# Optimization experiments

Hardware: AMD Instinct MI355X
Metric: run time of the kernel (lower is better)

The kernel has to match this reference:

```python
import jax, jax.numpy as jnp
import numpy as np

NUM_HEADS = 12
HEAD_DIM = 128
HIDDEN = 1536
SCALE = HEAD_DIM ** -0.5


def apply_rope(x, rope):
    # x: [B,H,S,D], rope: [S,1,D] -> freqs [S,D]
    freqs = rope[:, 0, :]
    cos = jnp.repeat(freqs[:, 0::2], 2, axis=-1)[None, None]  # [1,1,S,D]
    sin = jnp.repeat(freqs[:, 1::2], 2, axis=-1)[None, None]
    xr = x.reshape(*x.shape[:-1], -1, 2)
    x_real, x_imag = xr[..., 0], xr[..., 1]
    x_rot = jnp.stack([-x_imag, x_real], axis=-1).reshape(x.shape)
    return x * cos + x_rot * sin


def qkv_split(x, W):
    # x: [B,S,hidden], W: [3*H*D, hidden] (torch Linear layout)
    B, S, _ = x.shape
    y = (x @ W.T).reshape(B, S, 3, NUM_HEADS, HEAD_DIM).transpose(2, 0, 3, 1, 4)
    return y[0], y[1], y[2]  # each [B,H,S,D]


def sdpa(q, k, v):
    s = jnp.einsum('bhqd,bhkd->bhqk', q, k) * SCALE
    p = jax.nn.softmax(s, axis=-1)
    return jnp.einsum('bhqk,bhkd->bhqd', p, v)


def setup_inputs() -> dict:
    key = jax.random.key(0)
    ks = jax.random.split(key, 7)
    B, L, N = 1, 512, 4096
    txt = jax.random.normal(ks[0], (B, L, HIDDEN), dtype=jnp.float32)
    img = jax.random.normal(ks[1], (B, N, HIDDEN), dtype=jnp.float32)
    rope = jax.random.uniform(ks[2], (N, 1, HEAD_DIM), dtype=jnp.float32)
    s = 0.02
    W_txt_qkv = jax.random.normal(ks[3], (3 * NUM_HEADS * HEAD_DIM, HIDDEN), dtype=jnp.float32) * s
    W_img_qkv = jax.random.normal(ks[4], (3 * NUM_HEADS * HEAD_DIM, HIDDEN), dtype=jnp.float32) * s
    W_txt_out = jax.random.normal(ks[5], (HIDDEN, NUM_HEADS * HEAD_DIM), dtype=jnp.float32) * s
    W_img_out = jax.random.normal(ks[6], (HIDDEN, NUM_HEADS * HEAD_DIM), dtype=jnp.float32) * s
    return {'txt': txt, 'img': img, 'rope': rope, 'W_txt_qkv': W_txt_qkv,
            'W_img_qkv': W_img_qkv, 'W_txt_out': W_txt_out, 'W_img_out': W_img_out}


def reference(txt, img, rope, W_txt_qkv, W_img_qkv, W_txt_out, W_img_out):
    B, L, _ = txt.shape
    _, N, _ = img.shape
    txt_q, txt_k, txt_v = qkv_split(txt, W_txt_qkv)
    img_q, img_k, img_v = qkv_split(img, W_img_qkv)
    img_q = apply_rope(img_q, rope)
    img_k = apply_rope(img_k, rope)
    k = jnp.concatenate([txt_k, img_k], axis=2)  # [B,H,L+N,D]
    v = jnp.concatenate([txt_v, img_v], axis=2)
    txt_o = sdpa(txt_q, k, v).transpose(0, 2, 1, 3).reshape(B, L, -1)
    img_o = sdpa(img_q, k, v).transpose(0, 2, 1, 3).reshape(B, N, -1)
    return txt_o @ W_txt_out.T, img_o @ W_img_out.T
```

## Files before the change

### kernel.cpp

```cpp
#include <hip/hip_runtime.h>
#include <hip/hip_bf16.h>
#include <stdint.h>


typedef __attribute__((ext_vector_type(8)))  short bf16x8;
typedef __attribute__((ext_vector_type(4)))  float f32x4;
typedef __attribute__((ext_vector_type(16))) float f32x16;
typedef __attribute__((ext_vector_type(4)))  short s16x4;

#define NUM_HEADS 12
#define HEAD_DIM  128
#define HIDDEN    1536
#define LTXT      512
#define NIMG      4096
#define STOT      4608
#define QKV3      4608
#define SCALE_Q2  (0.08838834764831845f * 1.44269504088896340f)
#define DEFER_THR 12.0f

__device__ __forceinline__ float b2f(short s) {
    union { uint32_t u; float f; } c; c.u = ((uint32_t)(uint16_t)s) << 16; return c.f;
}
__device__ __forceinline__ short f2b(float f) {
    union { float f; uint32_t u; } c; c.f = f;
    uint32_t u = c.u + 0x7FFFu + ((c.u >> 16) & 1u);
    return (short)(u >> 16);
}
__device__ __forceinline__ float fexp2(float x) {
#if __has_builtin(__builtin_amdgcn_exp2f)
    return __builtin_amdgcn_exp2f(x);
#else
    return exp2f(x);
#endif
}
__device__ __forceinline__ uint32_t cvt_pk_bf16(float lo, float hi) {
    uint32_t r;
    asm("v_cvt_pk_bf16_f32 %0, %1, %2" : "=v"(r) : "v"(lo), "v"(hi));
    return r;
}
__device__ __forceinline__ void permlane32_swap(uint32_t& a, uint32_t& b) {
    asm("v_permlane32_swap_b32 %0, %1" : "+v"(a), "+v"(b));
}

typedef const void __attribute__((address_space(1)))* gas_p;
typedef void __attribute__((address_space(3)))* las_p;
__device__ __forceinline__ void gload_lds16(const void* g, void* l) {
    __builtin_amdgcn_global_load_lds((gas_p)g, (las_p)l, 16, 0, 0);
}

__global__ __launch_bounds__(256) void cast6(
    const float* __restrict__ s0, const float* __restrict__ s1,
    const float* __restrict__ s2, const float* __restrict__ s3,
    const float* __restrict__ s4, const float* __restrict__ s5,
    short* __restrict__ dst)
{
    size_t i = (size_t)blockIdx.x * 256 + threadIdx.x;
    const size_t e0 = 98304, e1 = 884736, e2 = 1769472,
                 e3 = 2654208, e4 = 2949120;
    const float* src; size_t base;
    if (i < e2) {
        if (i < e0)      { src = s0; base = 0;  }
        else if (i < e1) { src = s1; base = e0; }
        else             { src = s2; base = e1; }
    } else {
        if (i < e3)      { src = s3; base = e2; }
        else if (i < e4) { src = s4; base = e3; }
        else             { src = s5; base = e4; }
    }
    const float4* p = (const float4*)src + (i - base) * 2;
    float4 a = p[0], b = p[1];
    bf16x8 o;
    o[0] = f2b(a.x); o[1] = f2b(a.y); o[2] = f2b(a.z); o[3] = f2b(a.w);
    o[4] = f2b(b.x); o[5] = f2b(b.y); o[6] = f2b(b.z); o[7] = f2b(b.w);
    *((bf16x8*)dst + i) = o;
}

template <typename OT>
__global__ __launch_bounds__(256) void gemm_bt2(
    const short* __restrict__ A, const short* __restrict__ B0,
    const short* __restrict__ B1, OT* __restrict__ C,
    int M, int N, int K, int rowsplit)
{
    __shared__ __align__(16) short As[2][128 * 32];
    __shared__ __align__(16) short Bs[2][128 * 32];
    const int t    = threadIdx.x;
    const int lane = t & 63, wid = t >> 6;
    const int wr = wid >> 1, wc = wid & 1;
    const int l15 = lane & 15, lk = lane >> 4;
    const int bm = blockIdx.y, bn = blockIdx.x;

    const short* B = (bm * 128 < rowsplit) ? B0 : B1;
    const int srow = t >> 2, skg = t & 3;
    const short* Ag = A + (size_t)(bm * 128 + srow) * K + skg * 8;
    const short* Bg = B + (size_t)(bn * 128 + srow) * K + skg * 8;
    const size_t rowblk = (size_t)64 * K;

    f32x4 acc[4][4];
    const f32x4 z = {0.f, 0.f, 0.f, 0.f};
#pragma unroll
    for (int i = 0; i < 4; ++i)
#pragma unroll
        for (int j = 0; j < 4; ++j) acc[i][j] = z;

    auto STAGE = [&](int b, int kt) {
        const int k0 = kt * 32;
        gload_lds16(Ag + k0,          &As[b][wid * 512]);
        gload_lds16(Ag + rowblk + k0, &As[b][2048 + wid * 512]);
        gload_lds16(Bg + k0,          &Bs[b][wid * 512]);
        gload_lds16(Bg + rowblk + k0, &Bs[b][2048 + wid * 512]);
    };

    const int NT = K / 32;
    STAGE(0, 0);
    for (int kt = 0; kt < NT; ++kt) {
        const int cur = kt & 1;
        if (kt + 1 < NT) {
            STAGE(cur ^ 1, kt + 1);
            asm volatile("s_waitcnt vmcnt(4)" ::: "memory");
        } else {
            asm volatile("s_waitcnt vmcnt(0)" ::: "memory");
        }
        __builtin_amdgcn_s_barrier();

        bf16x8 af[4], bfr[4];
#pragma unroll
        for (int i = 0; i < 4; ++i)
            af[i] = *(const bf16x8*)&As[cur][(wr * 64 + i * 16 + l15) * 32 + lk * 8];
#pragma unroll
        for (int j = 0; j < 4; ++j)
            bfr[j] = *(const bf16x8*)&Bs[cur][(wc * 64 + j * 16 + l15) * 32 + lk * 8];
        __builtin_amdgcn_s_setprio(1);
#pragma unroll
        for (int i = 0; i < 4; ++i)
#pragma unroll
            for (int j = 0; j < 4; ++j)
                acc[i][j] = __builtin_amdgcn_mfma_f32_16x16x32_bf16(
                    af[i], bfr[j], acc[i][j], 0, 0, 0);
        __builtin_amdgcn_s_setprio(0);

        asm volatile("s_waitcnt lgkmcnt(0)" ::: "memory");
        __builtin_amdgcn_sched_barrier(0);
        __builtin_amdgcn_s_barrier();
    }

#pragma unroll
    for (int i = 0; i < 4; ++i) {
#pragma unroll
        for (int j = 0; j < 4; ++j) {
            const int row0 = bm * 128 + wr * 64 + i * 16 + lk * 4;
            const int col  = bn * 128 + wc * 64 + j * 16 + l15;
#pragma unroll
            for (int r = 0; r < 4; ++r) {
                float v = acc[i][j][r];
                if constexpr (sizeof(OT) == 2)
                    C[(size_t)(row0 + r) * N + col] = (OT)f2b(v);
                else
                    C[(size_t)(row0 + r) * N + col] = v;
            }
        }
    }
}

__global__ __launch_bounds__(256) void pack_qkv(
    const short* __restrict__ Y, const float* __restrict__ rope,
    short* __restrict__ Qb, short* __restrict__ Kb, short* __restrict__ VTb)
{
    const int st = blockIdx.x, h = blockIdx.y, t = threadIdx.x;
    const int s0 = st * 64;
    __shared__ __align__(16) short Vt[128][72];

#pragma unroll
    for (int i = 0; i < 4; ++i) {
        int e  = t + i * 256;
        int sl = e >> 4, dg = e & 15;
        int s  = s0 + sl;
        const short* src = Y + (size_t)s * QKV3;
        bf16x8 q8 = *(const bf16x8*)(src + h * 128 + dg * 8);
        bf16x8 k8 = *(const bf16x8*)(src + (12 + h) * 128 + dg * 8);
        bf16x8 v8 = *(const bf16x8*)(src + (24 + h) * 128 + dg * 8);
        float qf[8], kf[8];
#pragma unroll
        for (int j = 0; j < 8; ++j) { qf[j] = b2f(q8[j]); kf[j] = b2f(k8[j]); }
        if (s >= LTXT) {
            const float* rp = rope + (size_t)(s - LTXT) * 128 + dg * 8;
            float4 r0 = *(const float4*)rp;
            float4 r1 = *(const float4*)(rp + 4);
            float rr[8] = {r0.x, r0.y, r0.z, r0.w, r1.x, r1.y, r1.z, r1.w};
#pragma unroll
            for (int j = 0; j < 4; ++j) {
                float c = rr[2 * j], sn = rr[2 * j + 1];
                float q0 = qf[2 * j], q1 = qf[2 * j + 1];
                qf[2 * j] = q0 * c - q1 * sn; qf[2 * j + 1] = q1 * c + q0 * sn;
                float k0 = kf[2 * j], k1 = kf[2 * j + 1];
                kf[2 * j] = k0 * c - k1 * sn; kf[2 * j + 1] = k1 * c + k0 * sn;
            }
        }
        bf16x8 qo, ko;
#pragma unroll
        for (int j = 0; j < 8; ++j) { qo[j] = f2b(qf[j] * SCALE_Q2); ko[j] = f2b(kf[j]); }
        *(bf16x8*)(Qb + ((size_t)h * STOT + s) * 128 + dg * 8) = qo;
        *(bf16x8*)(Kb + ((size_t)h * STOT + s) * 128 + dg * 8) = ko;
#pragma unroll
        for (int j = 0; j < 8; ++j) Vt[dg * 8 + j][sl] = v8[j];
    }
    __syncthreads();
#pragma unroll
    for (int i = 0; i < 4; ++i) {
        int c = t + i * 256;
        int d = c >> 3, sg = c & 7;
        bf16x8 val = *(const bf16x8*)&Vt[d][sg * 8];
        *(bf16x8*)(VTb + ((size_t)h * 128 + d) * STOT + s0 + sg * 8) = val;
    }
}

__global__ __launch_bounds__(512, 2) void attn_fwd(
    const short* __restrict__ Q, const short* __restrict__ Kb,
    const short* __restrict__ VT, short* __restrict__ O)
{
    const int qb = blockIdx.x, h = blockIdx.y, t = threadIdx.x;
    const int lane = t & 63, wid = t >> 6;
    const int l31 = lane & 31, hi = lane >> 5;
    const int xorb = l31 & 7;

    __shared__ __align__(16) short Ks[2][64 * 128];
    __shared__ __align__(16) short Vs[2][64 * 128];

    const short* Qrow = Q + ((size_t)h * STOT + qb * 256 + wid * 32 + l31) * 128;
    bf16x8 qf[8];
#pragma unroll
    for (int dk = 0; dk < 8; ++dk)
        qf[dk] = *(const bf16x8*)(Qrow + dk * 16 + hi * 8);

    f32x16 o[4];
#pragma unroll
    for (int nt = 0; nt < 4; ++nt)
#pragma unroll
        for (int r = 0; r < 16; ++r) o[nt][r] = 0.f;
    float m = -1e30f, den = 0.f;

    const short* Kh = Kb + (size_t)h * STOT * 128;
    const short* Vh = VT + (size_t)h * 128 * STOT;

    const short* Ksrc[2]; const short* Vsrc[2];
    short* Kdst[2][2]; short* Vdst[2][2];
#pragma unroll
    for (int i = 0; i < 2; ++i) {
        int p = t + i * 512;
        int krow = p >> 4, kx = (p & 15) ^ (krow & 7);
        Ksrc[i] = Kh + (size_t)krow * 128 + kx * 8;
        int vrow = p >> 3, vx = (p & 7) ^ (vrow & 7);
        Vsrc[i] = Vh + (size_t)vrow * STOT + vx * 8;
#pragma unroll
        for (int b = 0; b < 2; ++b) {
            Kdst[b][i] = &Ks[b][i * 4096 + wid * 512];
            Vdst[b][i] = &Vs[b][i * 4096 + wid * 512];
        }
    }

    auto STAGE = [&](int b, int kb) {
#pragma unroll
        for (int i = 0; i < 2; ++i) {
            gload_lds16(Ksrc[i] + (size_t)kb * 8192, Kdst[b][i]);
            gload_lds16(Vsrc[i] + (size_t)kb * 64,   Vdst[b][i]);
        }
    };

    const int NT = STOT / 64;
    STAGE(0, 0);
    for (int kb = 0; kb < NT; ++kb) {
        const int cur = kb & 1;
        if (kb + 1 < NT) {
            STAGE(cur ^ 1, kb + 1);
            asm volatile("s_waitcnt vmcnt(4)" ::: "memory");
        } else {
            asm volatile("s_waitcnt vmcnt(0)" ::: "memory");
        }
        __builtin_amdgcn_s_barrier();

        const char* Ksc = (const char*)&Ks[cur][0];
        const char* Vsc = (const char*)&Vs[cur][0];

        f32x16 sc0, sc1;
#pragma unroll
        for (int r = 0; r < 16; ++r) { sc0[r] = 0.f; sc1[r] = 0.f; }
        __builtin_amdgcn_s_setprio(1);
#pragma unroll
        for (int dk = 0; dk < 8; ++dk) {
            bf16x8 kf0 = *(const bf16x8*)(Ksc + (l31)      * 256 + (((dk * 2 + hi) ^ xorb) << 4));
            bf16x8 kf1 = *(const bf16x8*)(Ksc + (32 + l31) * 256 + (((dk * 2 + hi) ^ xorb) << 4));
            sc0 = __builtin_amdgcn_mfma_f32_32x32x16_bf16(kf0, qf[dk], sc0, 0, 0, 0);
            sc1 = __builtin_amdgcn_mfma_f32_32x32x16_bf16(kf1, qf[dk], sc1, 0, 0, 0);
        }
        __builtin_amdgcn_s_setprio(0);

        float v = sc0[0];
#pragma unroll
        for (int r = 1; r < 16; ++r) v = fmaxf(v, sc0[r]);
#pragma unroll
        for (int r = 0; r < 16; ++r) v = fmaxf(v, sc1[r]);
        v = fmaxf(v, __shfl_xor(v, 32));
        if (__any(v > m + DEFER_THR)) {
            float mn = fmaxf(m, v);
            float al = fexp2(m - mn);
            m = mn;
            den *= al;
#pragma unroll
            for (int nt = 0; nt < 4; ++nt)
#pragma unroll
                for (int r = 0; r < 16; ++r) o[nt][r] *= al;
        }
        float rs = 0.f;
#pragma unroll
        for (int r = 0; r < 16; ++r) { sc0[r] = fexp2(sc0[r] - m); rs += sc0[r]; }
#pragma unroll
        for (int r = 0; r < 16; ++r) { sc1[r] = fexp2(sc1[r] - m); rs += sc1[r]; }
        rs += __shfl_xor(rs, 32);
        den += rs;

        __builtin_amdgcn_s_setprio(1);
#pragma unroll
        for (int s = 0; s < 4; ++s) {
            const f32x16& pe = (s < 2) ? sc0 : sc1;
            const int rb = (s & 1) * 8;
            uint32_t a0 = cvt_pk_bf16(pe[rb + 0], pe[rb + 1]);
            uint32_t a1 = cvt_pk_bf16(pe[rb + 2], pe[rb + 3]);
            uint32_t a2 = cvt_pk_bf16(pe[rb + 4], pe[rb + 5]);
            uint32_t a3 = cvt_pk_bf16(pe[rb + 6], pe[rb + 7]);
            permlane32_swap(a0, a2);
            permlane32_swap(a1, a3);
            union { uint32_t u[4]; bf16x8 v8; } pb;
            pb.u[0] = a0; pb.u[1] = a1; pb.u[2] = a2; pb.u[3] = a3;
#pragma unroll
            for (int nt = 0; nt < 4; ++nt) {
                bf16x8 vf = *(const bf16x8*)(Vsc + (nt * 32 + l31) * 128 +
                                             (((s * 2 + hi) ^ xorb) << 4));
                o[nt] = __builtin_amdgcn_mfma_f32_32x32x16_bf16(vf, pb.v8, o[nt], 0, 0, 0);
            }
        }
        __builtin_amdgcn_s_setprio(0);

        asm volatile("s_waitcnt lgkmcnt(0)" ::: "memory");
        __builtin_amdgcn_sched_barrier(0);
        __builtin_amdgcn_s_barrier();
    }

    const int qrow = qb * 256 + wid * 32 + l31;
    float inv = 1.0f / den;
    short* Orow = O + (size_t)qrow * HIDDEN + h * 128;
#pragma unroll
    for (int nt = 0; nt < 4; ++nt) {
#pragma unroll
        for (int g = 0; g < 4; ++g) {
            s16x4 w4;
#pragma unroll
            for (int j = 0; j < 4; ++j) w4[j] = f2b(o[nt][g * 4 + j] * inv);
            *(s16x4*)(Orow + nt * 32 + g * 8 + hi * 4) = w4;
        }
    }
}

extern "C" void kernel_launch(void* const* d_in, const int* in_sizes, int n_in,
                              void* d_out, int out_size, void* d_ws, size_t ws_size,
                              hipStream_t stream)
{
    (void)in_sizes; (void)n_in; (void)out_size; (void)ws_size;
    const float* txt  = (const float*)d_in[0];
    const float* img  = (const float*)d_in[1];
    const float* rope = (const float*)d_in[2];
    const float* Wtq  = (const float*)d_in[3];
    const float* Wiq  = (const float*)d_in[4];
    const float* Wto  = (const float*)d_in[5];
    const float* Wio  = (const float*)d_in[6];
    float* out = (float*)d_out;

    short* w = (short*)d_ws;
    size_t off = 0;
    auto alloc = [&](size_t elems) { short* p = w + off; off += elems; return p; };
    short* txtb = alloc((size_t)LTXT * HIDDEN);
    short* imgb = alloc((size_t)NIMG * HIDDEN);
    short* Wtqb = alloc((size_t)QKV3 * HIDDEN);
    short* Wiqb = alloc((size_t)QKV3 * HIDDEN);
    short* Wtob = alloc((size_t)HIDDEN * HIDDEN);
    short* Wiob = alloc((size_t)HIDDEN * HIDDEN);
    short* Yt   = alloc((size_t)LTXT * QKV3);
    short* Yi   = alloc((size_t)NIMG * QKV3);
    short* Qb   = alloc((size_t)NUM_HEADS * STOT * HEAD_DIM);
    short* Kb   = alloc((size_t)NUM_HEADS * STOT * HEAD_DIM);
    short* VTb  = alloc((size_t)NUM_HEADS * STOT * HEAD_DIM);
    (void)imgb; (void)Yi;
    short* Ob   = txtb;

    cast6<<<12672, 256, 0, stream>>>(txt, img, Wtq, Wiq, Wto, Wio, txtb);

    gemm_bt2<short><<<dim3(QKV3 / 128, STOT / 128), 256, 0, stream>>>(
        txtb, Wtqb, Wiqb, Yt, STOT, QKV3, HIDDEN, LTXT);

    pack_qkv<<<dim3(STOT / 64, NUM_HEADS), 256, 0, stream>>>(
        Yt, rope, Qb, Kb, VTb);

    attn_fwd<<<dim3(STOT / 256, NUM_HEADS), 512, 0, stream>>>(Qb, Kb, VTb, Ob);

    gemm_bt2<float><<<dim3(HIDDEN / 128, STOT / 128), 256, 0, stream>>>(
        Ob, Wtob, Wiob, out, STOT, HIDDEN, HIDDEN, LTXT);
}
```

Measured before the change: 320.5 us.

## Triple-buffer K/V tiles in attention and swizzle blocks across XCDs

The attention loop moves from double to triple LDS buffering, unrolled by three. This drops the trailing lgkmcnt wait and the second barrier each tile needed, leaving one barrier per tile and a deeper prefetch. A 1D grid with a swizzled block index puts the query blocks of one head on the same XCD, to improve L2 reuse of K/V. LDS swizzle addresses are also precomputed once. LDS per block grows from 64KB to 96KB, which limits residency to one block per CU; the grid of 216 blocks already fits on the CUs, so this mainly costs latency hiding.

```diff
diff --git a/kernel.cpp b/kernel.cpp
--- a/kernel.cpp
+++ b/kernel.cpp
@@ -217,13 +217,16 @@
     const short* __restrict__ Q, const short* __restrict__ Kb,
     const short* __restrict__ VT, short* __restrict__ O)
 {
-    const int qb = blockIdx.x, h = blockIdx.y, t = threadIdx.x;
+    const int id  = blockIdx.x;
+    const int swz = (id & 7) * 27 + (id >> 3);
+    const int qb  = swz % 18, h = swz / 18;
+
+    const int t = threadIdx.x;
     const int lane = t & 63, wid = t >> 6;
     const int l31 = lane & 31, hi = lane >> 5;
     const int xorb = l31 & 7;
 
-    __shared__ __align__(16) short Ks[2][64 * 128];
-    __shared__ __align__(16) short Vs[2][64 * 128];
+    __shared__ __align__(16) short KV[3][2][64 * 128];
 
     const short* Qrow = Q + ((size_t)h * STOT + qb * 256 + wid * 32 + l31) * 128;
     bf16x8 qf[8];
@@ -242,7 +245,6 @@
     const short* Vh = VT + (size_t)h * 128 * STOT;
 
     const short* Ksrc[2]; const short* Vsrc[2];
-    short* Kdst[2][2]; short* Vdst[2][2];
 #pragma unroll
     for (int i = 0; i < 2; ++i) {
         int p = t + i * 512;
@@ -250,44 +252,38 @@
         Ksrc[i] = Kh + (size_t)krow * 128 + kx * 8;
         int vrow = p >> 3, vx = (p & 7) ^ (vrow & 7);
         Vsrc[i] = Vh + (size_t)vrow * STOT + vx * 8;
-#pragma unroll
-        for (int b = 0; b < 2; ++b) {
-            Kdst[b][i] = &Ks[b][i * 4096 + wid * 512];
-            Vdst[b][i] = &Vs[b][i * 4096 + wid * 512];
-        }
     }
 
     auto STAGE = [&](int b, int kb) {
 #pragma unroll
         for (int i = 0; i < 2; ++i) {
-            gload_lds16(Ksrc[i] + (size_t)kb * 8192, Kdst[b][i]);
-            gload_lds16(Vsrc[i] + (size_t)kb * 64,   Vdst[b][i]);
+            gload_lds16(Ksrc[i] + (size_t)kb * 8192, &KV[b][0][i * 4096 + wid * 512]);
+            gload_lds16(Vsrc[i] + (size_t)kb * 64,   &KV[b][1][i * 4096 + wid * 512]);
         }
     };
 
-    const int NT = STOT / 64;
-    STAGE(0, 0);
-    for (int kb = 0; kb < NT; ++kb) {
-        const int cur = kb & 1;
-        if (kb + 1 < NT) {
-            STAGE(cur ^ 1, kb + 1);
-            asm volatile("s_waitcnt vmcnt(4)" ::: "memory");
-        } else {
-            asm volatile("s_waitcnt vmcnt(0)" ::: "memory");
-        }
-        __builtin_amdgcn_s_barrier();
-
-        const char* Ksc = (const char*)&Ks[cur][0];
-        const char* Vsc = (const char*)&Vs[cur][0];
-
+    int kaddr[8], vaddr[4];
+#pragma unroll
+    for (int dk = 0; dk < 8; ++dk)
+        kaddr[dk] = l31 * 256 + (((dk * 2 + hi) ^ xorb) << 4);
+#pragma unroll
+    for (int s = 0; s < 4; ++s)
+        vaddr[s] = l31 * 128 + (((s * 2 + hi) ^ xorb) << 4);
+
+    const char* Kbase[3] = { (const char*)&KV[0][0][0], (const char*)&KV[1][0][0],
+                             (const char*)&KV[2][0][0] };
+    const char* Vbase[3] = { (const char*)&KV[0][1][0], (const char*)&KV[1][1][0],
+                             (const char*)&KV[2][1][0] };
+
+    auto TILE = [&](const char* Ksc, const char* Vsc) {
         f32x16 sc0, sc1;
 #pragma unroll
         for (int r = 0; r < 16; ++r) { sc0[r] = 0.f; sc1[r] = 0.f; }
         __builtin_amdgcn_s_setprio(1);
 #pragma unroll
         for (int dk = 0; dk < 8; ++dk) {
-            bf16x8 kf0 = *(const bf16x8*)(Ksc + (l31)      * 256 + (((dk * 2 + hi) ^ xorb) << 4));
-            bf16x8 kf1 = *(const bf16x8*)(Ksc + (32 + l31) * 256 + (((dk * 2 + hi) ^ xorb) << 4));
+            bf16x8 kf0 = *(const bf16x8*)(Ksc + kaddr[dk]);
+            bf16x8 kf1 = *(const bf16x8*)(Ksc + kaddr[dk] + 8192);
             sc0 = __builtin_amdgcn_mfma_f32_32x32x16_bf16(kf0, qf[dk], sc0, 0, 0, 0);
             sc1 = __builtin_amdgcn_mfma_f32_32x32x16_bf16(kf1, qf[dk], sc1, 0, 0, 0);
         }
@@ -332,16 +328,34 @@
             pb.u[0] = a0; pb.u[1] = a1; pb.u[2] = a2; pb.u[3] = a3;
 #pragma unroll
             for (int nt = 0; nt < 4; ++nt) {
-                bf16x8 vf = *(const bf16x8*)(Vsc + (nt * 32 + l31) * 128 +
-                                             (((s * 2 + hi) ^ xorb) << 4));
+                bf16x8 vf = *(const bf16x8*)(Vsc + vaddr[s] + nt * 4096);
                 o[nt] = __builtin_amdgcn_mfma_f32_32x32x16_bf16(vf, pb.v8, o[nt], 0, 0, 0);
             }
         }
         __builtin_amdgcn_s_setprio(0);
-
-        asm volatile("s_waitcnt lgkmcnt(0)" ::: "memory");
-        __builtin_amdgcn_sched_barrier(0);
+    };
+
+    const int NT = STOT / 64;
+    STAGE(0, 0);
+    for (int kb3 = 0; kb3 < NT; kb3 += 3) {
+        STAGE(1, kb3 + 1);
+        asm volatile("s_waitcnt vmcnt(4)" ::: "memory");
         __builtin_amdgcn_s_barrier();
+        TILE(Kbase[0], Vbase[0]);
+
+        STAGE(2, kb3 + 2);
+        asm volatile("s_waitcnt vmcnt(4)" ::: "memory");
+        __builtin_amdgcn_s_barrier();
+        TILE(Kbase[1], Vbase[1]);
+
+        if (kb3 + 3 < NT) {
+            STAGE(0, kb3 + 3);
+            asm volatile("s_waitcnt vmcnt(4)" ::: "memory");
+        } else {
+            asm volatile("s_waitcnt vmcnt(0)" ::: "memory");
+        }
+        __builtin_amdgcn_s_barrier();
+        TILE(Kbase[2], Vbase[2]);
     }
 
     const int qrow = qb * 256 + wid * 32 + l31;
@@ -398,7 +412,7 @@
     pack_qkv<<<dim3(STOT / 64, NUM_HEADS), 256, 0, stream>>>(
         Yt, rope, Qb, Kb, VTb);
 
-    attn_fwd<<<dim3(STOT / 256, NUM_HEADS), 512, 0, stream>>>(Qb, Kb, VTb, Ob);
+    attn_fwd<<<dim3(STOT / 256 * NUM_HEADS), 512, 0, stream>>>(Qb, Kb, VTb, Ob);
 
     gemm_bt2<float><<<dim3(HIDDEN / 128, STOT / 128), 256, 0, stream>>>(
         Ob, Wtob, Wiob, out, STOT, HIDDEN, HIDDEN, LTXT);
```

Result: faster. 307.7 us (-4.0%).
